# Optimization experiments

Measured on AMD Instinct MI355X. Metric: run time of the kernel, lower is better.

Reference implementation:

```python
import jax, jax.numpy as jnp
import numpy as np

jax.config.update("jax_enable_x64", True)  # torch uses int64 labels with wrapping arithmetic

N = 100_000   # nodes
E = 3_200_000 # edges
D = 128       # label classes (argmax dim)
NUM_ITERATIONS = 3


def setup_inputs() -> dict:
    key = jax.random.key(0)
    k1, k2 = jax.random.split(key)
    x = jax.random.normal(k1, (N, D), dtype=jnp.float32)
    edge_index = jax.random.randint(k2, (2, E), 0, N, dtype=jnp.int64)
    return {"x": x, "edge_index": edge_index}


def _edge_exponents(row):
    """For each edge e, number of edges AFTER e (in edge order) sharing the same row.

    The torch loop computes neighborhood[r] = neighborhood[r]*31 + labels[c]
    sequentially over edges, i.e. for a row-group with targets c_1..c_k (edge order)
    the result is sum_j labels[c_j] * 31**(k - j). The exponent (k - j) is exactly
    the count of later same-row edges.
    """
    e = row.shape[0]
    order = jnp.argsort(row, stable=True)          # stable sort preserves edge order within groups
    srow = row[order]
    first = jnp.searchsorted(srow, srow, side="left")   # group start index
    last = jnp.searchsorted(srow, srow, side="right")   # group end index (exclusive)
    pos = jnp.arange(e) - first                          # position within group
    exp_sorted = (last - first) - 1 - pos                # edges remaining after this one
    return jnp.zeros(e, dtype=jnp.int64).at[order].set(exp_sorted)


def reference(x, edge_index):
    labels = jnp.argmax(x, axis=-1).astype(jnp.int64) if x.ndim > 1 else x.astype(jnp.int64)
    row, col = edge_index[0], edge_index[1]
    exps = _edge_exponents(row)
    # 31**exp in wrapping int64 arithmetic; exponentiation-by-squaring mod 2^64
    # matches the sequential multiply-add mod 2^64 of the torch loop.
    pow31 = jnp.power(jnp.int64(31), exps)
    history = [labels]
    for _ in range(NUM_ITERATIONS):
        vals = labels[col] * pow31                       # [E] per-edge weighted labels
        labels = jax.ops.segment_sum(vals, row, num_segments=N)  # ordered hash accumulate
        history.append(labels)
    return (labels, *history)
```

## Files before the change

### kernel.cpp

```cpp
#include <hip/hip_runtime.h>
#include <hip/hip_bf16.h>


#define WL_D 128
#define NCH 512
#define GRID_F 2048
#define BT 512
#define MSDW 8
#define BBITS 8
#define BROWS 256
#define NBK 512
#define RLSHIFT 23
#define COLMASK ((1u << RLSHIFT) - 1u)
#define CMAX 10240
#define NBMAX 13
#define HP8 2487512833u

template <int BITS>
__device__ inline unsigned long long match_key(unsigned v) {
    unsigned long long m = ~0ull;
    #pragma unroll
    for (int b = 0; b < BITS; ++b) {
        unsigned long long s = __ballot((v >> b) & 1u);
        m &= ((v >> b) & 1u) ? s : ~s;
    }
    return m;
}

__global__ void __launch_bounds__(BT)
k_hist_argmax(const float* __restrict__ x, const int* __restrict__ ei,
              unsigned* __restrict__ lab0, unsigned* __restrict__ hist,
              int N, int E, int chunk, int nbuckets) {
    __shared__ unsigned h[NBK];
    int b = blockIdx.x, t = threadIdx.x, lane = t & 63, w = t >> 6;
    if (b < NCH) {
        for (int i = t; i < nbuckets; i += BT) h[i] = 0u;
        __syncthreads();
        int base = b * chunk, lim = min(base + chunk, E);
        for (int e = base + t; e < lim; e += BT)
            atomicAdd(&h[((unsigned)ei[e]) >> BBITS], 1u);
        __syncthreads();
        for (int v = t; v < nbuckets; v += BT) hist[(size_t)v * NCH + b] = h[v];
    }
    int half = lane >> 5, li = lane & 31;
    for (int pr = b * MSDW + w; 2 * pr < N; pr += GRID_F * MSDW) {
        int r = 2 * pr + half;
        float bv = -3.4e38f; int bi = 0;
        if (r < N) {
            float4 v = ((const float4*)(x + (size_t)r * WL_D))[li];
            bv = v.x; bi = 4 * li;
            if (v.y > bv) { bv = v.y; bi = 4 * li + 1; }
            if (v.z > bv) { bv = v.z; bi = 4 * li + 2; }
            if (v.w > bv) { bv = v.w; bi = 4 * li + 3; }
        }
        #pragma unroll
        for (int off = 16; off > 0; off >>= 1) {
            float ov = __shfl_down(bv, off, 32);
            int   oi = __shfl_down(bi, off, 32);
            if (ov > bv || (ov == bv && oi < bi)) { bv = ov; bi = oi; }
        }
        if (li == 0 && r < N) lab0[r] = (unsigned)bi;
    }
}

__global__ void __launch_bounds__(BT)
k_scan_tile(unsigned* __restrict__ hist, unsigned* __restrict__ bsums, int L) {
    __shared__ unsigned smem[BT];
    int b = blockIdx.x, t = threadIdx.x;
    int i0 = b * 1024;
    unsigned v0 = (i0 + 2 * t     < L) ? hist[i0 + 2 * t]     : 0u;
    unsigned v1 = (i0 + 2 * t + 1 < L) ? hist[i0 + 2 * t + 1] : 0u;
    unsigned s = v0 + v1;
    smem[t] = s;
    __syncthreads();
    for (int o = 1; o < BT; o <<= 1) {
        unsigned u = (t >= o) ? smem[t - o] : 0u;
        __syncthreads();
        smem[t] += u;
        __syncthreads();
    }
    unsigned excl = smem[t] - s;
    if (i0 + 2 * t     < L) hist[i0 + 2 * t]     = excl;
    if (i0 + 2 * t + 1 < L) hist[i0 + 2 * t + 1] = excl + v0;
    if (t == BT - 1) bsums[b] = smem[BT - 1];
}

__global__ void __launch_bounds__(BT)
k_scan_sums(unsigned* __restrict__ bsums, int ntiles) {
    __shared__ unsigned smem[BT];
    int t = threadIdx.x;
    unsigned v = (t < ntiles) ? bsums[t] : 0u;
    smem[t] = v;
    __syncthreads();
    for (int o = 1; o < BT; o <<= 1) {
        unsigned u = (t >= o) ? smem[t - o] : 0u;
        __syncthreads();
        smem[t] += u;
        __syncthreads();
    }
    if (t < ntiles) bsums[t] = smem[t] - v;
}

__global__ void __launch_bounds__(BT)
k_transp(const unsigned* __restrict__ hist, const unsigned* __restrict__ bsums,
         unsigned* __restrict__ histT, int nbuckets) {
    __shared__ unsigned tl[64][65];
    int vtiles = (nbuckets + 63) / 64;
    int bx = blockIdx.x % vtiles;
    int by = blockIdx.x / vtiles;
    int tx = threadIdx.x & 63, ty = threadIdx.x >> 6;
    int v0 = bx * 64, b0 = by * 64;
    #pragma unroll
    for (int r = 0; r < 8; ++r) {
        int row = r * 8 + ty;
        int v = v0 + row;
        size_t idx = (size_t)v * NCH + (b0 + tx);
        tl[row][tx] = (v < nbuckets) ? (hist[idx] + bsums[idx >> 10]) : 0u;
    }
    __syncthreads();
    #pragma unroll
    for (int r = 0; r < 8; ++r) {
        int row = r * 8 + ty;
        int v = v0 + tx;
        if (v < nbuckets) histT[(size_t)(b0 + row) * nbuckets + v] = tl[tx][row];
    }
}

__global__ void __launch_bounds__(BT)
k_scatter(const int* __restrict__ ei, const unsigned* __restrict__ histT,
          unsigned* __restrict__ buf, int E, int chunk, int nbuckets) {
    __shared__ unsigned wbase[MSDW * NBK];
    int b = blockIdx.x, t = threadIdx.x, lane = t & 63, w = t >> 6;
    unsigned long long lmask = (1ull << lane) - 1ull;
    for (int i = t; i < MSDW * NBK; i += BT) wbase[i] = 0u;
    __syncthreads();
    int base = b * chunk, lim = min(base + chunk, E);
    int sub  = (chunk + MSDW - 1) / MSDW;
    int wbeg = base + w * sub;
    int wend = min(wbeg + sub, lim);
    int nbat = (wbeg < wend) ? ((wend - wbeg + 63) >> 6) : 0;
    unsigned r_[NBMAX];
    #pragma unroll
    for (int k = 0; k < NBMAX; ++k) {
        int e = wbeg + k * 64 + lane;
        r_[k] = (e < wend) ? (unsigned)ei[e] : 0u;
    }
    #pragma unroll
    for (int k = 0; k < NBMAX; ++k) {
        if (k >= nbat) break;
        int e = wbeg + k * 64 + lane;
        bool act = (e < wend);
        unsigned v = act ? (r_[k] >> BBITS) : (NBK - 1u);
        unsigned long long m = match_key<9>(v);
        unsigned before = (unsigned)__popcll(m & lmask);
        unsigned total  = (unsigned)__popcll(m);
        if (act && before == 0u) wbase[w * NBK + v] += total;
    }
    for (int k = NBMAX; k < nbat; ++k) {
        int e = wbeg + k * 64 + lane;
        bool act = (e < wend);
        unsigned v = act ? (((unsigned)ei[e]) >> BBITS) : (NBK - 1u);
        unsigned long long m = match_key<9>(v);
        unsigned before = (unsigned)__popcll(m & lmask);
        unsigned total  = (unsigned)__popcll(m);
        if (act && before == 0u) wbase[w * NBK + v] += total;
    }
    __syncthreads();
    for (int v = t; v < nbuckets; v += BT) {
        unsigned g = histT[(size_t)b * nbuckets + v];
        #pragma unroll
        for (int w2 = 0; w2 < MSDW; ++w2) {
            unsigned cnt = wbase[w2 * NBK + v];
            wbase[w2 * NBK + v] = g;
            g += cnt;
        }
    }
    __syncthreads();
    unsigned c_[NBMAX];
    #pragma unroll
    for (int k = 0; k < NBMAX; ++k) {
        int e = wbeg + k * 64 + lane;
        c_[k] = (e < wend) ? (unsigned)ei[(size_t)E + e] : 0u;
    }
    #pragma unroll
    for (int k = 0; k < NBMAX; ++k) {
        if (k >= nbat) break;
        int e = wbeg + k * 64 + lane;
        bool act = (e < wend);
        unsigned r = r_[k], col = c_[k];
        unsigned v = act ? (r >> BBITS) : (NBK - 1u);
        unsigned long long m = match_key<9>(v);
        unsigned before = (unsigned)__popcll(m & lmask);
        unsigned total  = (unsigned)__popcll(m);
        int leader = __ffsll(m) - 1;
        unsigned base0 = 0;
        if (act && before == 0u) { base0 = wbase[w * NBK + v]; wbase[w * NBK + v] = base0 + total; }
        base0 = __shfl(base0, leader, 64);
        if (act) buf[base0 + before] = ((r & (BROWS - 1u)) << RLSHIFT) | col;
    }
    for (int k = NBMAX; k < nbat; ++k) {
        int e = wbeg + k * 64 + lane;
        bool act = (e < wend);
        unsigned r   = act ? (unsigned)ei[e] : 0u;
        unsigned col = act ? (unsigned)ei[(size_t)E + e] : 0u;
        unsigned v = act ? (r >> BBITS) : (NBK - 1u);
        unsigned long long m = match_key<9>(v);
        unsigned before = (unsigned)__popcll(m & lmask);
        unsigned total  = (unsigned)__popcll(m);
        int leader = __ffsll(m) - 1;
        unsigned base0 = 0;
        if (act && before == 0u) { base0 = wbase[w * NBK + v]; wbase[w * NBK + v] = base0 + total; }
        base0 = __shfl(base0, leader, 64);
        if (act) buf[base0 + before] = ((r & (BROWS - 1u)) << RLSHIFT) | col;
    }
}

__global__ void __launch_bounds__(BT)
k_bucket(const unsigned* __restrict__ buf, const unsigned* __restrict__ hist,
         const unsigned* __restrict__ bsums, unsigned* __restrict__ csr,
         unsigned* __restrict__ rs_g, int N, int E, int nbuckets) {
    __shared__ unsigned data2[CMAX];
    __shared__ unsigned h2[MSDW * BROWS];
    __shared__ unsigned offs[BROWS];
    int bb = blockIdx.x, t = threadIdx.x, lane = t & 63, w = t >> 6;
    unsigned long long lmask = (1ull << lane) - 1ull;
    size_t i0 = (size_t)bb * NCH;
    unsigned start = hist[i0] + bsums[i0 >> 10];
    unsigned end;
    if (bb + 1 < nbuckets) { size_t i1 = (size_t)(bb + 1) * NCH; end = hist[i1] + bsums[i1 >> 10]; }
    else end = (unsigned)E;
    unsigned len = end - start;
    bool lds_ok = (len <= CMAX);
    for (int i = t; i < MSDW * BROWS; i += BT) h2[i] = 0u;
    __syncthreads();
    unsigned sub  = (len + MSDW - 1u) / MSDW;
    unsigned wbeg = w * sub;
    unsigned wend = min(wbeg + sub, len);
    int nbat = (wbeg < wend) ? (int)((wend - wbeg + 63u) >> 6) : 0;
    for (int bt2 = 0; bt2 < nbat; ++bt2) {
        unsigned i = wbeg + (unsigned)(bt2 * 64 + lane);
        bool act = (i < wend);
        unsigned v = act ? (buf[start + i] >> RLSHIFT) : 511u;
        unsigned long long m = match_key<9>(v);
        unsigned before = (unsigned)__popcll(m & lmask);
        unsigned total  = (unsigned)__popcll(m);
        if (act && before == 0u) h2[w * BROWS + v] += total;
    }
    __syncthreads();
    unsigned hv = 0;
    if (t < BROWS) {
        #pragma unroll
        for (int w2 = 0; w2 < MSDW; ++w2) hv += h2[w2 * BROWS + t];
        offs[t] = hv;
    }
    __syncthreads();
    for (int o = 1; o < BROWS; o <<= 1) {
        unsigned s = (t < BROWS && t >= o) ? offs[t - o] : 0u;
        __syncthreads();
        if (t < BROWS) offs[t] += s;
        __syncthreads();
    }
    if (t < BROWS) {
        unsigned excl = offs[t] - hv;
        int row = bb * BROWS + t;
        if (row < N) rs_g[row] = start + excl;
        unsigned g = lds_ok ? excl : (start + excl);
        #pragma unroll
        for (int w2 = 0; w2 < MSDW; ++w2) {
            unsigned cnt = h2[w2 * BROWS + t];
            h2[w2 * BROWS + t] = g;
            g += cnt;
        }
    }
    __syncthreads();
    for (int bt2 = 0; bt2 < nbat; ++bt2) {
        unsigned i = wbeg + (unsigned)(bt2 * 64 + lane);
        bool act = (i < wend);
        unsigned p = act ? buf[start + i] : 0u;
        unsigned v = act ? (p >> RLSHIFT) : 511u;
        unsigned long long m = match_key<9>(v);
        unsigned before = (unsigned)__popcll(m & lmask);
        unsigned total  = (unsigned)__popcll(m);
        int leader = __ffsll(m) - 1;
        unsigned base0 = 0;
        if (act && before == 0u) { base0 = h2[w * BROWS + v]; h2[w * BROWS + v] = base0 + total; }
        base0 = __shfl(base0, leader, 64);
        if (act) {
            if (lds_ok) data2[base0 + before] = p & COLMASK;
            else        csr[base0 + before]   = p & COLMASK;
        }
    }
    __syncthreads();
    if (lds_ok) for (unsigned i = t; i < len; i += BT) csr[start + i] = data2[i];
}

__device__ inline unsigned horner8(const unsigned* __restrict__ csr,
                                   const unsigned* __restrict__ rs,
                                   const unsigned* __restrict__ lin,
                                   int g, int l, int N, int E) {
    unsigned s = rs[g];
    unsigned e = (g + 1 < N) ? rs[g + 1] : (unsigned)E;
    unsigned d = e - s;
    unsigned h = 0u;
    unsigned M = (d > (unsigned)l) ? ((d - (unsigned)l + 7u) >> 3) : 0u;
    for (unsigned m = 0; m < M; ++m) {
        unsigned col = csr[s + (unsigned)l + 8u * m];
        h = h * HP8 + lin[col];
    }
    if (M) {
        unsigned T = d - 1u - (unsigned)l - 8u * (M - 1u);
        unsigned p = ((T & 1u) ? 31u : 1u) * ((T & 2u) ? 961u : 1u)
                   * ((T & 4u) ? 923521u : 1u);
        h *= p;
    }
    h += __shfl_xor(h, 1, 64);
    h += __shfl_xor(h, 2, 64);
    h += __shfl_xor(h, 4, 64);
    return h;
}

__global__ void __launch_bounds__(BT)
k_prop(const unsigned* __restrict__ csr, const unsigned* __restrict__ rs,
       const unsigned* __restrict__ lin, unsigned* __restrict__ lout,
       int N, int E) {
    int idx = blockIdx.x * BT + threadIdx.x;
    int g = idx >> 3, l = idx & 7;
    if (g >= N) return;
    unsigned h = horner8(csr, rs, lin, g, l, N, E);
    if (l == 0) lout[g] = h;
}

__global__ void __launch_bounds__(BT)
k_prop_final(const unsigned* __restrict__ csr, const unsigned* __restrict__ rs,
             const unsigned* __restrict__ lin, const unsigned* __restrict__ l0,
             const unsigned* __restrict__ l1, int* __restrict__ out,
             int N, int E, int pgrid) {
    int idx = blockIdx.x * BT + threadIdx.x;
    int g = idx >> 3, l = idx & 7;
    if (g < N) {
        unsigned h = horner8(csr, rs, lin, g, l, N, E);
        if (l == 0) { out[g] = (int)h; out[4 * N + g] = (int)h; }
    }
    for (int i = idx; i < N; i += pgrid * BT) {
        out[N + i]     = (int)l0[i];
        out[2 * N + i] = (int)l1[i];
        out[3 * N + i] = (int)lin[i];
    }
}

extern "C" void kernel_launch(void* const* d_in, const int* in_sizes, int n_in,
                              void* d_out, int out_size, void* d_ws, size_t ws_size,
                              hipStream_t stream) {
    const float* x  = (const float*)d_in[0];
    const int*   ei = (const int*)d_in[1];
    int* out = (int*)d_out;

    int N = in_sizes[0] / WL_D;
    int E = in_sizes[1] / 2;
    int chunk    = (E + NCH - 1) / NCH;
    int nbuckets = (N + BROWS - 1) / BROWS;
    int L        = nbuckets * NCH;
    int ntiles   = (L + 1023) / 1024;
    int vtiles   = (nbuckets + 63) / 64;
    int btiles   = NCH / 64;
    int pgrid    = (8 * N + BT - 1) / BT;

    unsigned* ws   = (unsigned*)d_ws;
    unsigned* lab0 = ws;
    unsigned* lab1 = lab0 + N;
    unsigned* lab2 = lab1 + N;
    unsigned* rs   = lab2 + N;
    unsigned* bs   = rs + N;
    unsigned* hist = bs + 1024;
    unsigned* buf  = hist + L;
    unsigned* csr  = buf + E;
    unsigned* histT = csr;

    k_hist_argmax<<<GRID_F, BT, 0, stream>>>(x, ei, lab0, hist, N, E, chunk, nbuckets);
    k_scan_tile<<<ntiles, BT, 0, stream>>>(hist, bs, L);
    k_scan_sums<<<1, BT, 0, stream>>>(bs, ntiles);
    k_transp<<<vtiles * btiles, BT, 0, stream>>>(hist, bs, histT, nbuckets);
    k_scatter<<<NCH, BT, 0, stream>>>(ei, histT, buf, E, chunk, nbuckets);
    k_bucket<<<nbuckets, BT, 0, stream>>>(buf, hist, bs, csr, rs, N, E, nbuckets);
    k_prop<<<pgrid, BT, 0, stream>>>(csr, rs, lab0, lab1, N, E);
    k_prop<<<pgrid, BT, 0, stream>>>(csr, rs, lab1, lab2, N, E);
    k_prop_final<<<pgrid, BT, 0, stream>>>(csr, rs, lab2, lab0, lab1, out, N, E, pgrid);
}
```

Baseline: 216.6 us.

## Fuse first propagation into bucket kernel and scan-sums into transpose

```diff
diff --git a/kernel.cpp b/kernel.cpp
--- a/kernel.cpp
+++ b/kernel.cpp
@@ -86,44 +86,47 @@
 }
 
 __global__ void __launch_bounds__(BT)
-k_scan_sums(unsigned* __restrict__ bsums, int ntiles) {
-    __shared__ unsigned smem[BT];
+k_transp(const unsigned* __restrict__ hist, const unsigned* __restrict__ bsums,
+         unsigned* __restrict__ histT, unsigned* __restrict__ bstart,
+         int nbuckets, int ntiles, int E) {
+    __shared__ unsigned tl[64][65];
+    __shared__ unsigned sb[BT];
     int t = threadIdx.x;
-    unsigned v = (t < ntiles) ? bsums[t] : 0u;
-    smem[t] = v;
+    unsigned my = (t < ntiles) ? bsums[t] : 0u;
+    sb[t] = my;
     __syncthreads();
     for (int o = 1; o < BT; o <<= 1) {
-        unsigned u = (t >= o) ? smem[t - o] : 0u;
-        __syncthreads();
-        smem[t] += u;
-        __syncthreads();
-    }
-    if (t < ntiles) bsums[t] = smem[t] - v;
-}
-
-__global__ void __launch_bounds__(BT)
-k_transp(const unsigned* __restrict__ hist, const unsigned* __restrict__ bsums,
-         unsigned* __restrict__ histT, int nbuckets) {
-    __shared__ unsigned tl[64][65];
+        unsigned u = (t >= o) ? sb[t - o] : 0u;
+        __syncthreads();
+        sb[t] += u;
+        __syncthreads();
+    }
+    sb[t] -= my;
+    __syncthreads();
     int vtiles = (nbuckets + 63) / 64;
     int bx = blockIdx.x % vtiles;
     int by = blockIdx.x / vtiles;
-    int tx = threadIdx.x & 63, ty = threadIdx.x >> 6;
-    int v0 = bx * 64, b0 = by * 64;
+    int tx = t & 63, ty = t >> 6;
+    int vb = bx * 64, b0 = by * 64;
     #pragma unroll
     for (int r = 0; r < 8; ++r) {
         int row = r * 8 + ty;
-        int v = v0 + row;
+        int v = vb + row;
         size_t idx = (size_t)v * NCH + (b0 + tx);
-        tl[row][tx] = (v < nbuckets) ? (hist[idx] + bsums[idx >> 10]) : 0u;
+        tl[row][tx] = (v < nbuckets) ? (hist[idx] + sb[idx >> 10]) : 0u;
     }
     __syncthreads();
     #pragma unroll
     for (int r = 0; r < 8; ++r) {
         int row = r * 8 + ty;
-        int v = v0 + tx;
+        int v = vb + tx;
         if (v < nbuckets) histT[(size_t)(b0 + row) * nbuckets + v] = tl[tx][row];
     }
+    if (by == 0 && t < 64) {
+        int v = vb + t;
+        if (v < nbuckets) bstart[v] = tl[t][0];
+    }
+    if (blockIdx.x == 0 && t == 64) bstart[nbuckets] = (unsigned)E;
 }
 
 __global__ void __launch_bounds__(BT)
@@ -145,6 +148,7 @@
         int e = wbeg + k * 64 + lane;
         r_[k] = (e < wend) ? (unsigned)ei[e] : 0u;
     }
+    unsigned long long m_[NBMAX];
     #pragma unroll
     for (int k = 0; k < NBMAX; ++k) {
         if (k >= nbat) break;
@@ -152,9 +156,9 @@
         bool act = (e < wend);
         unsigned v = act ? (r_[k] >> BBITS) : (NBK - 1u);
         unsigned long long m = match_key<9>(v);
-        unsigned before = (unsigned)__popcll(m & lmask);
-        unsigned total  = (unsigned)__popcll(m);
-        if (act && before == 0u) wbase[w * NBK + v] += total;
+        m_[k] = m;
+        unsigned before = (unsigned)__popcll(m & lmask);
+        if (act && before == 0u) wbase[w * NBK + v] += (unsigned)__popcll(m);
     }
     for (int k = NBMAX; k < nbat; ++k) {
         int e = wbeg + k * 64 + lane;
@@ -162,8 +166,7 @@
         unsigned v = act ? (((unsigned)ei[e]) >> BBITS) : (NBK - 1u);
         unsigned long long m = match_key<9>(v);
         unsigned before = (unsigned)__popcll(m & lmask);
-        unsigned total  = (unsigned)__popcll(m);
-        if (act && before == 0u) wbase[w * NBK + v] += total;
+        if (act && before == 0u) wbase[w * NBK + v] += (unsigned)__popcll(m);
     }
     __syncthreads();
     for (int v = t; v < nbuckets; v += BT) {
@@ -188,6 +191,23 @@
         int e = wbeg + k * 64 + lane;
         bool act = (e < wend);
         unsigned r = r_[k], col = c_[k];
+        unsigned v = r >> BBITS;
+        unsigned long long m = m_[k];
+        unsigned before = (unsigned)__popcll(m & lmask);
+        int leader = __ffsll(m) - 1;
+        unsigned base0 = 0;
+        if (act && before == 0u) {
+            base0 = wbase[w * NBK + v];
+            wbase[w * NBK + v] = base0 + (unsigned)__popcll(m);
+        }
+        base0 = __shfl(base0, leader, 64);
+        if (act) buf[base0 + before] = ((r & (BROWS - 1u)) << RLSHIFT) | col;
+    }
+    for (int k = NBMAX; k < nbat; ++k) {
+        int e = wbeg + k * 64 + lane;
+        bool act = (e < wend);
+        unsigned r   = act ? (unsigned)ei[e] : 0u;
+        unsigned col = act ? (unsigned)ei[(size_t)E + e] : 0u;
         unsigned v = act ? (r >> BBITS) : (NBK - 1u);
         unsigned long long m = match_key<9>(v);
         unsigned before = (unsigned)__popcll(m & lmask);
@@ -198,37 +218,20 @@
         base0 = __shfl(base0, leader, 64);
         if (act) buf[base0 + before] = ((r & (BROWS - 1u)) << RLSHIFT) | col;
     }
-    for (int k = NBMAX; k < nbat; ++k) {
-        int e = wbeg + k * 64 + lane;
-        bool act = (e < wend);
-        unsigned r   = act ? (unsigned)ei[e] : 0u;
-        unsigned col = act ? (unsigned)ei[(size_t)E + e] : 0u;
-        unsigned v = act ? (r >> BBITS) : (NBK - 1u);
-        unsigned long long m = match_key<9>(v);
-        unsigned before = (unsigned)__popcll(m & lmask);
-        unsigned total  = (unsigned)__popcll(m);
-        int leader = __ffsll(m) - 1;
-        unsigned base0 = 0;
-        if (act && before == 0u) { base0 = wbase[w * NBK + v]; wbase[w * NBK + v] = base0 + total; }
-        base0 = __shfl(base0, leader, 64);
-        if (act) buf[base0 + before] = ((r & (BROWS - 1u)) << RLSHIFT) | col;
-    }
-}
-
-__global__ void __launch_bounds__(BT)
-k_bucket(const unsigned* __restrict__ buf, const unsigned* __restrict__ hist,
-         const unsigned* __restrict__ bsums, unsigned* __restrict__ csr,
-         unsigned* __restrict__ rs_g, int N, int E, int nbuckets) {
+}
+
+__global__ void __launch_bounds__(BT)
+k_bucket(const unsigned* __restrict__ buf, const unsigned* __restrict__ bstart,
+         unsigned* __restrict__ csr, unsigned* __restrict__ rs_g,
+         const unsigned* __restrict__ lab0, unsigned* __restrict__ lab1,
+         int N, int E, int nbuckets) {
     __shared__ unsigned data2[CMAX];
     __shared__ unsigned h2[MSDW * BROWS];
     __shared__ unsigned offs[BROWS];
     int bb = blockIdx.x, t = threadIdx.x, lane = t & 63, w = t >> 6;
     unsigned long long lmask = (1ull << lane) - 1ull;
-    size_t i0 = (size_t)bb * NCH;
-    unsigned start = hist[i0] + bsums[i0 >> 10];
-    unsigned end;
-    if (bb + 1 < nbuckets) { size_t i1 = (size_t)(bb + 1) * NCH; end = hist[i1] + bsums[i1 >> 10]; }
-    else end = (unsigned)E;
+    unsigned start = bstart[bb];
+    unsigned end   = bstart[bb + 1];
     unsigned len = end - start;
     bool lds_ok = (len <= CMAX);
     for (int i = t; i < MSDW * BROWS; i += BT) h2[i] = 0u;
@@ -291,6 +294,29 @@
         }
     }
     __syncthreads();
+    const unsigned* srcp = lds_ok ? (const unsigned*)data2 : (csr + start);
+    int l = t & 7;
+    for (int r0 = t >> 3; r0 < BROWS; r0 += BT / 8) {
+        unsigned beg = r0 ? offs[r0 - 1] : 0u;
+        unsigned d   = offs[r0] - beg;
+        unsigned h = 0u;
+        unsigned M = (d > (unsigned)l) ? ((d - (unsigned)l + 7u) >> 3) : 0u;
+        for (unsigned m = 0; m < M; ++m) {
+            unsigned col = srcp[beg + (unsigned)l + 8u * m];
+            h = h * HP8 + lab0[col];
+        }
+        if (M) {
+            unsigned T = d - 1u - (unsigned)l - 8u * (M - 1u);
+            unsigned p = ((T & 1u) ? 31u : 1u) * ((T & 2u) ? 961u : 1u)
+                       * ((T & 4u) ? 923521u : 1u);
+            h *= p;
+        }
+        h += __shfl_xor(h, 1, 64);
+        h += __shfl_xor(h, 2, 64);
+        h += __shfl_xor(h, 4, 64);
+        int row = bb * BROWS + r0;
+        if (l == 0 && row < N) lab1[row] = h;
+    }
     if (lds_ok) for (unsigned i = t; i < len; i += BT) csr[start + i] = data2[i];
 }
 
@@ -365,24 +391,23 @@
     int btiles   = NCH / 64;
     int pgrid    = (8 * N + BT - 1) / BT;
 
-    unsigned* ws   = (unsigned*)d_ws;
-    unsigned* lab0 = ws;
-    unsigned* lab1 = lab0 + N;
-    unsigned* lab2 = lab1 + N;
-    unsigned* rs   = lab2 + N;
-    unsigned* bs   = rs + N;
-    unsigned* hist = bs + 1024;
-    unsigned* buf  = hist + L;
-    unsigned* csr  = buf + E;
+    unsigned* ws    = (unsigned*)d_ws;
+    unsigned* lab0  = ws;
+    unsigned* lab1  = lab0 + N;
+    unsigned* lab2  = lab1 + N;
+    unsigned* rs    = lab2 + N;
+    unsigned* bs    = rs + N;
+    unsigned* bstart= bs + 1024;
+    unsigned* hist  = bstart + 1024;
+    unsigned* buf   = hist + L;
+    unsigned* csr   = buf + E;
     unsigned* histT = csr;
 
     k_hist_argmax<<<GRID_F, BT, 0, stream>>>(x, ei, lab0, hist, N, E, chunk, nbuckets);
     k_scan_tile<<<ntiles, BT, 0, stream>>>(hist, bs, L);
-    k_scan_sums<<<1, BT, 0, stream>>>(bs, ntiles);
-    k_transp<<<vtiles * btiles, BT, 0, stream>>>(hist, bs, histT, nbuckets);
+    k_transp<<<vtiles * btiles, BT, 0, stream>>>(hist, bs, histT, bstart, nbuckets, ntiles, E);
     k_scatter<<<NCH, BT, 0, stream>>>(ei, histT, buf, E, chunk, nbuckets);
-    k_bucket<<<nbuckets, BT, 0, stream>>>(buf, hist, bs, csr, rs, N, E, nbuckets);
-    k_prop<<<pgrid, BT, 0, stream>>>(csr, rs, lab0, lab1, N, E);
+    k_bucket<<<nbuckets, BT, 0, stream>>>(buf, bstart, csr, rs, lab0, lab1, N, E, nbuckets);
     k_prop<<<pgrid, BT, 0, stream>>>(csr, rs, lab1, lab2, N, E);
     k_prop_final<<<pgrid, BT, 0, stream>>>(csr, rs, lab2, lab0, lab1, out, N, E, pgrid);
 }
```

Result: faster. 209.1 us (-3.5%).
